# Performance work log

Measured on AMD Instinct MI355X. Metric: run time of the kernel, lower is better.

The kernel has to match this reference:

```python
import jax, jax.numpy as jnp
from jax import lax
import numpy as np

FEA = 256
NHEADS = 8
GROUPS = 32
SCALE = 1.0 / np.sqrt(FEA // NHEADS)  # 1/sqrt(qkv_dim//nheads)


def conv2d(x, w, b=None, pad=0, groups=1):
    out = lax.conv_general_dilated(
        x, w, (1, 1), [(pad, pad), (pad, pad)],
        dimension_numbers=("NCHW", "OIHW", "NCHW"),
        feature_group_count=groups)
    return out if b is None else out + b[None, :, None, None]


def group_norm(x, w, b, groups=GROUPS, eps=1e-5):
    B, C, H, W = x.shape
    xg = x.reshape(B, groups, C // groups, H, W)
    m = xg.mean(axis=(2, 3, 4), keepdims=True)
    v = xg.var(axis=(2, 3, 4), keepdims=True)
    xg = (xg - m) * lax.rsqrt(v + eps)
    return xg.reshape(B, C, H, W) * w[None, :, None, None] + b[None, :, None, None]


def l2norm(x, eps=1e-12):  # F.normalize over channel dim
    n = jnp.sqrt(jnp.sum(x * x, axis=1, keepdims=True))
    return x / jnp.maximum(n, eps)


def attn_op(q, k, v):
    b, c, xf, yf = q.shape
    sp = lambda t: t.reshape(b, NHEADS, c // NHEADS, xf * yf)
    q, k, v = sp(q), sp(k), sp(v)
    sim = jnp.einsum("bhjn,bhkn->bhjk", q, k) * SCALE  # channel attention, [b,h,c/h,c/h]
    sim = jax.nn.softmax(sim, axis=-1)
    out = jnp.einsum("bhjk,bhkn->bhjn", sim, v)
    return out.reshape(b, c, xf, yf)


def freqca(x, gn_w, gn_b, dw_w, pw_w, pw_b, ao_w, ao_b, f1_w, f2_w, f3_w, f3_b):
    H, W = x.shape[-2:]
    x = group_norm(x, gn_w, gn_b)
    qkv = conv2d(conv2d(x, dw_w, pad=1, groups=FEA), pw_w, pw_b)  # depthwise 3x3 then 1x1 -> 3*qkv_dim
    q, k, v = jnp.split(qkv, 3, axis=1)
    q, k, v = l2norm(q), l2norm(k), l2norm(v)
    qf = jnp.fft.rfft2(q, axes=(-2, -1), norm="ortho")
    kf = jnp.fft.rfft2(k, axes=(-2, -1), norm="ortho")
    vf = jnp.fft.rfft2(v, axes=(-2, -1), norm="ortho")
    amp = attn_op(jnp.abs(qf), jnp.abs(kf), jnp.abs(vf))
    phas = attn_op(jnp.angle(qf), jnp.angle(kf), jnp.angle(vf))
    out_c = amp * jnp.cos(phas) + 1j * (amp * jnp.sin(phas))  # torch.polar
    out = jnp.fft.irfft2(out_c, s=(H, W), axes=(-2, -1), norm="ortho")
    attn = conv2d(out, ao_w, ao_b) + x  # attn_res is Identity (fea_dim == dim_out)
    h = jax.nn.silu(conv2d(attn, f1_w, pad=1))
    h = conv2d(h, f2_w, pad=1)
    h = conv2d(h, f3_w, f3_b)
    return h + attn  # DropPath in eval mode = identity


def setup_inputs() -> dict:
    key = jax.random.key(0)
    ks = jax.random.split(key, 12)
    B, C, H, W = 8, FEA, 128, 128
    s = 0.02
    return {
        "x": jax.random.normal(ks[0], (B, C, H, W), jnp.float32),
        "gn_w": jnp.ones((C,), jnp.float32),
        "gn_b": jnp.zeros((C,), jnp.float32),
        "dw_w": jax.random.normal(ks[1], (C, 1, 3, 3), jnp.float32) * s,
        "pw_w": jax.random.normal(ks[2], (3 * C, C, 1, 1), jnp.float32) * s,
        "pw_b": jnp.zeros((3 * C,), jnp.float32),
        "ao_w": jax.random.normal(ks[3], (C, C, 1, 1), jnp.float32) * s,
        "ao_b": jnp.zeros((C,), jnp.float32),
        "f1_w": jax.random.normal(ks[4], (2 * C, C, 3, 3), jnp.float32) * s,
        "f2_w": jax.random.normal(ks[5], (C, 2 * C, 3, 3), jnp.float32) * s,
        "f3_w": jax.random.normal(ks[6], (C, C, 1, 1), jnp.float32) * s,
        "f3_b": jnp.zeros((C,), jnp.float32),
    }


def reference(x, gn_w, gn_b, dw_w, pw_w, pw_b, ao_w, ao_b, f1_w, f2_w, f3_w, f3_b):
    return freqca(x, gn_w, gn_b, dw_w, pw_w, pw_b, ao_w, ao_b, f1_w, f2_w, f3_w, f3_b)
```

## Files before the change

kernel.cpp:

```cpp
#include <hip/hip_runtime.h>
#include <hip/hip_bf16.h>
#include <math.h>


#define TWO_PI_D 6.283185307179586476925286766559
#define ATTN_SCALE 0.17677669529663687f

typedef __attribute__((ext_vector_type(8))) short short8;
typedef __attribute__((ext_vector_type(4))) short short4v;
typedef __attribute__((ext_vector_type(4))) float f32x4;
typedef _Float16 half8v __attribute__((ext_vector_type(8)));

__device__ inline short f2bf(float f) {
    __hip_bfloat16 h = __float2bfloat16(f);
    return *reinterpret_cast<short*>(&h);
}
__device__ inline unsigned short h_bits(_Float16 h) {
    union { _Float16 h; unsigned short u; } c; c.h = h; return c.u;
}

__global__ __launch_bounds__(256) void groupnorm_kernel(
    const float* __restrict__ x, const float* __restrict__ gw,
    const float* __restrict__ gb, float* __restrict__ out, int b0)
{
    int t = threadIdx.x;
    int lb = blockIdx.x >> 5;
    int g  = blockIdx.x & 31;
    size_t src = ((size_t)(b0 + lb) * 32 + g) * 131072;
    size_t dst = (size_t)blockIdx.x * 131072;
    const float* xp = x + src;
    double s = 0.0, ss = 0.0;
    for (int i = t; i < 131072; i += 256) { double v = xp[i]; s += v; ss += v*v; }
    __shared__ double rs[256], rss[256];
    rs[t] = s; rss[t] = ss;
    __syncthreads();
    for (int k = 128; k > 0; k >>= 1) {
        if (t < k) { rs[t] += rs[t+k]; rss[t] += rss[t+k]; }
        __syncthreads();
    }
    __shared__ float smean, sinv;
    if (t == 0) {
        double mean = rs[0] * (1.0/131072.0);
        double var  = rss[0] * (1.0/131072.0) - mean*mean;
        smean = (float)mean;
        sinv  = (float)(1.0 / sqrt(var + 1e-5));
    }
    __syncthreads();
    float mean = smean, inv = sinv;
    for (int i = t; i < 131072; i += 256) {
        int c = (g << 3) + (i >> 14);
        out[dst + i] = (xp[i] - mean) * inv * gw[c] + gb[c];
    }
}

__global__ __launch_bounds__(256) void dwconv_kernel(
    const float* __restrict__ in, const float* __restrict__ w, float* __restrict__ out)
{
    int t = threadIdx.x;
    int bc = blockIdx.x >> 6;
    int ystrip = (blockIdx.x & 63) << 1;
    int c  = bc & 255;
    const float* wp = w + c*9;
    const float* ip = in + ((size_t)bc << 14);
    __shared__ float xs[4][128];
    for (int i = t; i < 512; i += 256) {
        int rr = i >> 7, xx = i & 127;
        int yy = ystrip - 1 + rr;
        xs[rr][xx] = (yy >= 0 && yy < 128) ? ip[(yy << 7) + xx] : 0.f;
    }
    __syncthreads();
    int r0 = t >> 7;
    int x  = t & 127;
    float acc = 0.f;
    #pragma unroll
    for (int dy = 0; dy < 3; dy++) {
        const float* row = xs[r0 + dy];
        #pragma unroll
        for (int dx = 0; dx < 3; dx++) {
            int xx = x + dx - 1;
            if (xx >= 0 && xx <= 127) acc += wp[dy*3+dx] * row[xx];
        }
    }
    out[((size_t)bc << 14) + ((ystrip + r0) << 7) + x] = acc;
}

__global__ __launch_bounds__(256) void wcvtpw_kernel(
    const float* __restrict__ w, _Float16* __restrict__ whi,
    _Float16* __restrict__ wlo, int total)
{
    int i = blockIdx.x * 256 + threadIdx.x;
    if (i >= total) return;
    float v = w[i];
    _Float16 h = (_Float16)v;
    _Float16 l = (_Float16)(v - (float)h);
    whi[i] = h; wlo[i] = l;
}

__global__ __launch_bounds__(256) void twcvt_kernel(
    _Float16* __restrict__ twh, _Float16* __restrict__ twl)
{
    int i = blockIdx.x * 256 + threadIdx.x;
    if (i >= 20480) return;
    int bin = i >> 7, w = i & 127;
    double v = 0.0;
    if (bin < 65) v = cos(TWO_PI_D * ((bin * w) & 127) / 128.0) * 0.0078125;
    else if (bin < 130) v = -sin(TWO_PI_D * (((bin - 65) * w) & 127) / 128.0) * 0.0078125;
    _Float16 h = (_Float16)v;
    twh[i] = h;
    twl[i] = (_Float16)((float)v - (float)h);
}

__global__ __launch_bounds__(256) void micvt_kernel(
    _Float16* __restrict__ mih, _Float16* __restrict__ mil)
{
    int i = blockIdx.x * 256 + threadIdx.x;
    if (i >= 65536) return;
    int row = i >> 8, col = i & 255;
    int k1 = col >> 1, u = col & 1;
    int yy = row & 127;
    double ang = TWO_PI_D * ((k1 * yy) & 127) / 128.0;
    double cc = cos(ang), sn = sin(ang);
    double v;
    if (row < 128) v = (u == 0) ? cc : -sn;
    else           v = (u == 0) ? sn :  cc;
    _Float16 h = (_Float16)v;
    mih[i] = h;
    mil[i] = (_Float16)((float)v - (float)h);
}

__global__ __launch_bounds__(256) void convpw_kernel(
    const float* __restrict__ in, const _Float16* __restrict__ whi,
    const _Float16* __restrict__ wlo, const float* __restrict__ bias,
    float* __restrict__ out)
{
    int y      = blockIdx.x;
    int coBase = blockIdx.y << 7;
    int lb     = blockIdx.z;
    int t = threadIdx.x;
    int lane = t & 63;
    int wave = t >> 6;
    int wm = (wave >> 1) << 6;
    int wn = (wave & 1) << 6;
    int lr = lane & 15;
    int kg = (lane >> 4) << 3;

    __shared__ _Float16 Ah[128][40], Al[128][40];
    __shared__ _Float16 Bh[128][40], Bl[128][40];

    f32x4 acc[4][4];
    #pragma unroll
    for (int i = 0; i < 4; i++)
        #pragma unroll
        for (int j = 0; j < 4; j++) acc[i][j] = (f32x4){0.f, 0.f, 0.f, 0.f};

    const float* inrow = in + (((size_t)lb * 256) << 14) + (y << 7);
    for (int ci0 = 0; ci0 < 256; ci0 += 32) {
        __syncthreads();
        #pragma unroll
        for (int u = 0; u < 2; u++) {
            int ii = t + (u << 8);
            int co = ii >> 2, cg = ii & 3;
            *(half8v*)&Ah[co][cg << 3] =
                *(const half8v*)&whi[(size_t)(coBase + co) * 256 + ci0 + (cg << 3)];
            *(half8v*)&Al[co][cg << 3] =
                *(const half8v*)&wlo[(size_t)(coBase + co) * 256 + ci0 + (cg << 3)];
        }
        for (int i = t; i < 2048; i += 256) {
            int px = i & 127, chp = i >> 7;
            int ci = ci0 + (chp << 1);
            float v0 = inrow[((size_t)ci << 14) + px];
            float v1 = inrow[((size_t)(ci + 1) << 14) + px];
            _Float16 h0 = (_Float16)v0, h1 = (_Float16)v1;
            _Float16 l0 = (_Float16)(v0 - (float)h0);
            _Float16 l1 = (_Float16)(v1 - (float)h1);
            unsigned uh = (unsigned)h_bits(h0) | ((unsigned)h_bits(h1) << 16);
            unsigned ul = (unsigned)h_bits(l0) | ((unsigned)h_bits(l1) << 16);
            *(unsigned*)&Bh[px][chp << 1] = uh;
            *(unsigned*)&Bl[px][chp << 1] = ul;
        }
        __syncthreads();
        half8v ah[4], al[4], bh4[4], bl4[4];
        #pragma unroll
        for (int i = 0; i < 4; i++) {
            ah[i] = *(const half8v*)&Ah[wm + i*16 + lr][kg];
            al[i] = *(const half8v*)&Al[wm + i*16 + lr][kg];
        }
        #pragma unroll
        for (int j = 0; j < 4; j++) {
            bh4[j] = *(const half8v*)&Bh[wn + j*16 + lr][kg];
            bl4[j] = *(const half8v*)&Bl[wn + j*16 + lr][kg];
        }
        #pragma unroll
        for (int i = 0; i < 4; i++)
            #pragma unroll
            for (int j = 0; j < 4; j++) {
                acc[i][j] = __builtin_amdgcn_mfma_f32_16x16x32_f16(
                    ah[i], bh4[j], acc[i][j], 0, 0, 0);
                acc[i][j] = __builtin_amdgcn_mfma_f32_16x16x32_f16(
                    ah[i], bl4[j], acc[i][j], 0, 0, 0);
                acc[i][j] = __builtin_amdgcn_mfma_f32_16x16x32_f16(
                    al[i], bh4[j], acc[i][j], 0, 0, 0);
            }
    }

    int pBase = y << 7;
    int mr = (lane >> 4) << 2;
    #pragma unroll
    for (int i = 0; i < 4; i++) {
        int co0 = coBase + wm + i*16 + mr;
        #pragma unroll
        for (int j = 0; j < 4; j++) {
            int px = pBase + wn + j*16 + lr;
            #pragma unroll
            for (int r = 0; r < 4; r++) {
                out[(((size_t)(lb*768 + co0 + r)) << 14) + px] =
                    acc[i][j][r] + bias[co0 + r];
            }
        }
    }
}

__global__ __launch_bounds__(256) void l2inv_kernel(
    const float* __restrict__ qkv, float* __restrict__ invn)
{
    int p  = ((blockIdx.x & 63) << 8) + threadIdx.x;
    int bT = blockIdx.x >> 6;
    int lb = bT / 3, T = bT - 3*lb;
    const float* base = qkv + (((size_t)(lb*768 + T*256)) << 14) + p;
    double ss = 0.0;
    for (int c = 0; c < 256; c++) { double v = base[(size_t)c << 14]; ss += v*v; }
    invn[((size_t)bT << 14) + p] = 1.f / fmaxf((float)sqrt(ss), 1e-12f);
}

__global__ __launch_bounds__(256) void fftrow_mfma_kernel(
    const float* __restrict__ qkv, const float* __restrict__ invn,
    const _Float16* __restrict__ twh, const _Float16* __restrict__ twl,
    float* __restrict__ rre, float* __restrict__ rim, int chunkBase)
{
    int loc = blockIdx.x;
    int gp  = chunkBase + loc;
    int t = threadIdx.x;
    int lane = t & 63;
    int wave = t >> 6;
    int wm  = (wave >> 1) << 6;
    int wnn = (wave & 1) * 80;
    int lr = lane & 15;
    int kq = (lane >> 4) << 3;

    __shared__ _Float16 Xh[128][68], Xl[128][68];

    int lb = gp / 768, chn = gp - lb*768, T = chn >> 8;
    const float4* src = (const float4*)(qkv + ((size_t)gp << 14));
    const float4* ivp = (const float4*)(invn + (((size_t)(lb*3 + T)) << 14));

    f32x4 acc[4][5];
    #pragma unroll
    for (int i = 0; i < 4; i++)
        #pragma unroll
        for (int j = 0; j < 5; j++) acc[i][j] = (f32x4){0.f, 0.f, 0.f, 0.f};

    for (int half = 0; half < 2; half++) {
        __syncthreads();
        for (int i = t; i < 2048; i += 256) {
            int r = i >> 4, q4 = i & 15;
            int gi = (r << 5) + (half << 4) + q4;
            float4 v = src[gi], w = ivp[gi];
            v.x *= w.x; v.y *= w.y; v.z *= w.z; v.w *= w.w;
            int cl = q4 << 2;
            _Float16 h0 = (_Float16)v.x, h1 = (_Float16)v.y;
            _Float16 h2 = (_Float16)v.z, h3 = (_Float16)v.w;
            Xh[r][cl+0] = h0; Xh[r][cl+1] = h1; Xh[r][cl+2] = h2; Xh[r][cl+3] = h3;
            Xl[r][cl+0] = (_Float16)(v.x - (float)h0);
            Xl[r][cl+1] = (_Float16)(v.y - (float)h1);
            Xl[r][cl+2] = (_Float16)(v.z - (float)h2);
            Xl[r][cl+3] = (_Float16)(v.w - (float)h3);
        }
        __syncthreads();
        #pragma unroll
        for (int ks = 0; ks < 2; ks++) {
            int k0 = (ks << 5) + kq;
            int kg = (half << 6) + k0;
            half8v ah[4], al[4], bh[5], bl[5];
            #pragma unroll
            for (int i = 0; i < 4; i++) {
                ah[i] = *(const half8v*)&Xh[wm + i*16 + lr][k0];
                al[i] = *(const half8v*)&Xl[wm + i*16 + lr][k0];
            }
            #pragma unroll
            for (int j = 0; j < 5; j++) {
                int bin = wnn + j*16 + lr;
                bh[j] = *(const half8v*)&twh[(size_t)bin * 128 + kg];
                bl[j] = *(const half8v*)&twl[(size_t)bin * 128 + kg];
            }
            #pragma unroll
            for (int i = 0; i < 4; i++)
                #pragma unroll
                for (int j = 0; j < 5; j++) {
                    acc[i][j] = __builtin_amdgcn_mfma_f32_16x16x32_f16(
                        ah[i], bh[j], acc[i][j], 0, 0, 0);
                    acc[i][j] = __builtin_amdgcn_mfma_f32_16x16x32_f16(
                        al[i], bh[j], acc[i][j], 0, 0, 0);
                    acc[i][j] = __builtin_amdgcn_mfma_f32_16x16x32_f16(
                        ah[i], bl[j], acc[i][j], 0, 0, 0);
                }
        }
    }

    int mr = (lane >> 4) << 2;
    #pragma unroll
    for (int i = 0; i < 4; i++) {
        #pragma unroll
        for (int j = 0; j < 5; j++) {
            int bin = wnn + j*16 + lr;
            if (bin < 130) {
                float* dst = (bin < 65) ? rre : rim;
                int bb = (bin < 65) ? bin : bin - 65;
                #pragma unroll
                for (int r = 0; r < 4; r++) {
                    int row = wm + i*16 + mr + r;
                    dst[((size_t)loc*128 + row)*65 + bb] = acc[i][j][r];
                }
            }
        }
    }
}

__global__ __launch_bounds__(256) void fft_col_kernel(
    const float* __restrict__ rre, const float* __restrict__ rim,
    float* __restrict__ spec, int chunkBase, size_t slotStride)
{
    int kb  = blockIdx.x * 13;
    int loc = blockIdx.y;
    int gp  = chunkBase + loc;
    int t   = threadIdx.x;
    __shared__ float zr[128][14], zi[128][14];
    __shared__ float gr[8][16][14], gi[8][16][14];
    __shared__ float ct[128], st[128];
    if (t < 128) { double s, c; sincos(TWO_PI_D * t / 128.0, &s, &c);
                   st[t] = (float)s; ct[t] = (float)c; }
    for (int i = t; i < 1664; i += 256) {
        int r = i / 13, k = i - r*13;
        size_t si = ((size_t)loc*128 + r)*65 + kb + k;
        zr[r][k] = rre[si];
        zi[r][k] = rim[si];
    }
    __syncthreads();
    for (int i = t; i < 1664; i += 256) {
        int kx = i % 13, rm = i / 13;
        int r0 = rm >> 4, m = rm & 15;
        int step = (m << 3) & 127;
        float gre = 0.f, gim = 0.f;
        int idx = 0;
        for (int r1 = 0; r1 < 16; r1++) {
            float cc = ct[idx], sn = st[idx];
            float a = zr[(r1 << 3) + r0][kx], b = zi[(r1 << 3) + r0][kx];
            gre += a*cc + b*sn;
            gim += b*cc - a*sn;
            idx = (idx + step) & 127;
        }
        gr[r0][m][kx] = gre;
        gi[r0][m][kx] = gim;
    }
    __syncthreads();
    int lb = gp / 768; int chn = gp - lb*768;
    int T = chn >> 8;  int c = chn & 255;
    float* aD = spec + (size_t)(2*T)   * slotStride + ((size_t)(lb*256 + c))*8320;
    float* pD = spec + (size_t)(2*T+1) * slotStride + ((size_t)(lb*256 + c))*8320;
    for (int i = t; i < 1664; i += 256) {
        int kx = i % 13, k1 = i / 13;
        int m = k1 & 15;
        float re = 0.f, im = 0.f;
        int idx = 0;
        for (int r0 = 0; r0 < 8; r0++) {
            float cc = ct[idx], sn = st[idx];
            float a = gr[r0][m][kx], b = gi[r0][m][kx];
            re += a*cc + b*sn;
            im += b*cc - a*sn;
            idx = (idx + k1) & 127;
        }
        int kxv = kb + kx;
        if ((k1 == 0 || k1 == 64) && (kxv == 0 || kxv == 64)) im = 0.f;
        int oi = k1*65 + kxv;
        aD[oi] = sqrtf(re*re + im*im);
        pD[oi] = atan2f(im, re);
    }
}

__global__ __launch_bounds__(256) void attn_sim_kernel(
    const float* __restrict__ qA, const float* __restrict__ kA,
    float* __restrict__ simpart)
{
    int sp = blockIdx.x;
    int bh = blockIdx.y;
    int lb = bh >> 3, h = bh & 7;
    int t = threadIdx.x;
    __shared__ float qs[32][132], ks[32][132];
    const float* qb = qA + ((size_t)(lb*256 + h*32)) * 8320;
    const float* kb = kA + ((size_t)(lb*256 + h*32)) * 8320;
    float acc[4] = {0.f, 0.f, 0.f, 0.f};
    int j0 = t >> 5;
    int kq = t & 31;
    for (int sub = 0; sub < 4; sub++) {
        int n0 = sp*520 + sub*130;
        __syncthreads();
        for (int i = t; i < 4160; i += 256) {
            int j = i / 130, nn = i - j*130;
            qs[j][nn] = qb[(size_t)j*8320 + n0 + nn];
            ks[j][nn] = kb[(size_t)j*8320 + n0 + nn];
        }
        __syncthreads();
        for (int nn = 0; nn < 128; nn += 4) {
            float4 kv = *(const float4*)&ks[kq][nn];
            #pragma unroll
            for (int e = 0; e < 4; e++) {
                float4 qv = *(const float4*)&qs[j0 + e*8][nn];
                acc[e] += qv.x*kv.x + qv.y*kv.y + qv.z*kv.z + qv.w*kv.w;
            }
        }
        {
            float2 kv = *(const float2*)&ks[kq][128];
            #pragma unroll
            for (int e = 0; e < 4; e++) {
                float2 qv = *(const float2*)&qs[j0 + e*8][128];
                acc[e] += qv.x*kv.x + qv.y*kv.y;
            }
        }
    }
    float* dst = simpart + ((size_t)bh*16 + sp) * 1024;
    dst[t]       = acc[0];
    dst[t + 256] = acc[1];
    dst[t + 512] = acc[2];
    dst[t + 768] = acc[3];
}

__global__ __launch_bounds__(256) void attn_out_kernel(
    const float* __restrict__ simpart, const float* __restrict__ vA,
    float* __restrict__ outA)
{
    int nb = blockIdx.x << 8;
    int bh = blockIdx.y;
    int lb = bh >> 3, h = bh & 7;
    int t = threadIdx.x;
    __shared__ float sim[32][32];
    for (int e = t; e < 1024; e += 256) {
        float s = 0.f;
        const float* pp = simpart + (size_t)bh*16384 + e;
        #pragma unroll
        for (int sp = 0; sp < 16; sp++) s += pp[sp*1024];
        sim[e >> 5][e & 31] = s * ATTN_SCALE;
    }
    __syncthreads();
    if (t < 32) {
        float m = -1e30f;
        for (int k = 0; k < 32; k++) m = fmaxf(m, sim[t][k]);
        float s = 0.f;
        for (int k = 0; k < 32; k++) s += expf(sim[t][k] - m);
        float inv = 1.f / s;
        for (int k = 0; k < 32; k++) sim[t][k] = expf(sim[t][k] - m) * inv;
    }
    __syncthreads();
    int n = nb + t;
    if (n >= 8320) return;
    const float* vb = vA + ((size_t)(lb*256 + h*32)) * 8320 + n;
    float vv[32];
    #pragma unroll
    for (int k = 0; k < 32; k++) vv[k] = vb[(size_t)k * 8320];
    float* ob = outA + ((size_t)(lb*256 + h*32)) * 8320 + n;
    for (int j = 0; j < 32; j++) {
        float o = 0.f;
        #pragma unroll
        for (int k = 0; k < 32; k++) o += sim[j][k] * vv[k];
        ob[(size_t)j * 8320] = o;
    }
}

__global__ __launch_bounds__(256) void ifftcol_mfma_kernel(
    const float* __restrict__ ampo, const float* __restrict__ pho,
    const _Float16* __restrict__ mih, const _Float16* __restrict__ mil,
    float* __restrict__ tre, float* __restrict__ tim)
{
    int plane = blockIdx.x;
    int t = threadIdx.x;
    int lane = t & 63;
    int wave = t >> 6;
    int wm = wave << 6;
    int lr = lane & 15;
    int kg = (lane >> 4) << 3;

    __shared__ _Float16 Bh[80][72], Bl[80][72];

    const float* ab = ampo + (size_t)plane * 8320;
    const float* pb = pho  + (size_t)plane * 8320;

    f32x4 acc[4][5];
    #pragma unroll
    for (int i = 0; i < 4; i++)
        #pragma unroll
        for (int j = 0; j < 5; j++) acc[i][j] = (f32x4){0.f, 0.f, 0.f, 0.f};

    for (int kc = 0; kc < 4; kc++) {
        __syncthreads();
        for (int i = t; i < 2080; i += 256) {
            int k1l = i / 65, kx = i - k1l*65;
            int k1 = (kc << 5) + k1l;
            float a = ab[k1*65 + kx];
            float p = pb[k1*65 + kx];
            float sp, cp; sincosf(p, &sp, &cp);
            float zr = a * cp, zi = a * sp;
            _Float16 hr = (_Float16)zr, hi = (_Float16)zi;
            unsigned uh = (unsigned)h_bits(hr) | ((unsigned)h_bits(hi) << 16);
            unsigned ul = (unsigned)h_bits((_Float16)(zr - (float)hr))
                        | ((unsigned)h_bits((_Float16)(zi - (float)hi)) << 16);
            *(unsigned*)&Bh[kx][k1l << 1] = uh;
            *(unsigned*)&Bl[kx][k1l << 1] = ul;
        }
        __syncthreads();
        #pragma unroll
        for (int ks = 0; ks < 2; ks++) {
            int kq = (ks << 5) + kg;
            int kgl = (kc << 6) + kq;
            half8v ah[4], al[4], bh[5], bl[5];
            #pragma unroll
            for (int i = 0; i < 4; i++) {
                int row = wm + i*16 + lr;
                ah[i] = *(const half8v*)&mih[(size_t)row * 256 + kgl];
                al[i] = *(const half8v*)&mil[(size_t)row * 256 + kgl];
            }
            #pragma unroll
            for (int j = 0; j < 5; j++) {
                int col = j*16 + lr;
                bh[j] = *(const half8v*)&Bh[col][kq];
                bl[j] = *(const half8v*)&Bl[col][kq];
            }
            #pragma unroll
            for (int i = 0; i < 4; i++)
                #pragma unroll
                for (int j = 0; j < 5; j++) {
                    acc[i][j] = __builtin_amdgcn_mfma_f32_16x16x32_f16(
                        ah[i], bh[j], acc[i][j], 0, 0, 0);
                    acc[i][j] = __builtin_amdgcn_mfma_f32_16x16x32_f16(
                        al[i], bh[j], acc[i][j], 0, 0, 0);
                    acc[i][j] = __builtin_amdgcn_mfma_f32_16x16x32_f16(
                        ah[i], bl[j], acc[i][j], 0, 0, 0);
                }
        }
    }

    int mr = (lane >> 4) << 2;
    #pragma unroll
    for (int i = 0; i < 4; i++) {
        #pragma unroll
        for (int j = 0; j < 5; j++) {
            int col = j*16 + lr;
            if (col < 65) {
                #pragma unroll
                for (int r = 0; r < 4; r++) {
                    int row = wm + i*16 + mr + r;
                    if (row < 128)
                        tre[((size_t)plane*128 + row)*65 + col] = acc[i][j][r];
                    else
                        tim[((size_t)plane*128 + (row - 128))*65 + col] = acc[i][j][r];
                }
            }
        }
    }
}

__global__ __launch_bounds__(256) void ifft_row_kernel(
    const float* __restrict__ tre, const float* __restrict__ tim,
    float* __restrict__ spat)
{
    int rc    = blockIdx.x;
    int plane = blockIdx.y;
    int t     = threadIdx.x;
    __shared__ float tr[16][66], ti[16][66];
    __shared__ float ct[128], st[128];
    if (t < 128) { double s, c; sincos(TWO_PI_D * t / 128.0, &s, &c);
                   st[t] = (float)s; ct[t] = (float)c; }
    for (int i = t; i < 1040; i += 256) {
        int r = i / 65, k = i - r*65;
        size_t si = ((size_t)plane*128 + rc*16 + r)*65 + k;
        float sc = (k >= 1 && k < 64) ? 2.f : 1.f;
        tr[r][k] = tre[si] * sc;
        ti[r][k] = tim[si] * sc;
    }
    __syncthreads();
    for (int oo = t; oo < 260; oo += 256) {
        int x = oo % 65, rq = oo / 65;
        int r0i = rq << 2;
        float C0 = tr[r0i+0][0], C1 = tr[r0i+1][0], C2 = tr[r0i+2][0], C3 = tr[r0i+3][0];
        float S0 = 0.f, S1 = 0.f, S2 = 0.f, S3 = 0.f;
        int m = x;
        for (int k = 1; k <= 64; k++) {
            float cc = ct[m], sn = st[m];
            C0 += tr[r0i+0][k]*cc; S0 += ti[r0i+0][k]*sn;
            C1 += tr[r0i+1][k]*cc; S1 += ti[r0i+1][k]*sn;
            C2 += tr[r0i+2][k]*cc; S2 += ti[r0i+2][k]*sn;
            C3 += tr[r0i+3][k]*cc; S3 += ti[r0i+3][k]*sn;
            m = (m + x) & 127;
        }
        size_t ob = ((size_t)plane << 14) + ((rc*16 + r0i) << 7);
        spat[ob + x]       = (C0 - S0)*0.0078125f;
        spat[ob + 128 + x] = (C1 - S1)*0.0078125f;
        spat[ob + 256 + x] = (C2 - S2)*0.0078125f;
        spat[ob + 384 + x] = (C3 - S3)*0.0078125f;
        if (x >= 1 && x <= 63) {
            int xm = 128 - x;
            spat[ob + xm]       = (C0 + S0)*0.0078125f;
            spat[ob + 128 + xm] = (C1 + S1)*0.0078125f;
            spat[ob + 256 + xm] = (C2 + S2)*0.0078125f;
            spat[ob + 384 + xm] = (C3 + S3)*0.0078125f;
        }
    }
}

__global__ __launch_bounds__(256) void wcvt_kernel(
    const float* __restrict__ w, short* __restrict__ wbf,
    int Cout, int Cin, int RR)
{
    int i = blockIdx.x * 256 + threadIdx.x;
    int total = Cout * Cin * RR;
    if (i >= total) return;
    int rr = i % RR;
    int ci = (i / RR) % Cin;
    int co = i / (RR * Cin);
    wbf[((size_t)rr * Cout + co) * Cin + ci] = f2bf(w[i]);
}

__global__ __launch_bounds__(256) void convmf2_kernel(
    const float* __restrict__ in, const short* __restrict__ wbf,
    const float* __restrict__ bias, const float* __restrict__ res,
    float* __restrict__ out, short* __restrict__ out_t,
    int Cin, int Cout, int act, int in_b0, int res_b0, int out_b0)
{
    int y      = blockIdx.x;
    int coBase = blockIdx.y << 7;
    int lb = blockIdx.z;
    int t = threadIdx.x;
    int lane = t & 63;
    int wave = t >> 6;
    int wm = (wave >> 1) << 6;
    int wn = (wave & 1) << 6;

    __shared__ short As[128][40];
    __shared__ short Bs[128][40];

    f32x4 acc[4][4];
    #pragma unroll
    for (int i = 0; i < 4; i++)
        #pragma unroll
        for (int j = 0; j < 4; j++) acc[i][j] = (f32x4){0.f, 0.f, 0.f, 0.f};

    const size_t inb = ((size_t)(in_b0 + lb) * Cin) << 14;
    int lr = lane & 15;
    int kg = (lane >> 4) << 3;

    const float* inrow = in + inb + (y << 7);
    const short* wslice = wbf + (size_t)coBase * Cin;
    for (int ci0 = 0; ci0 < Cin; ci0 += 32) {
        __syncthreads();
        #pragma unroll
        for (int u = 0; u < 2; u++) {
            int ii = t + (u << 8);
            int co = ii >> 2, cg = ii & 3;
            *(short8*)&As[co][cg << 3] =
                *(const short8*)&wslice[(size_t)co * Cin + ci0 + (cg << 3)];
        }
        for (int i = t; i < 2048; i += 256) {
            int px = i & 127, chp = i >> 7;
            int ci = ci0 + (chp << 1);
            float v0 = inrow[((size_t)ci << 14) + px];
            float v1 = inrow[((size_t)(ci + 1) << 14) + px];
            unsigned u2 = (unsigned)(unsigned short)f2bf(v0)
                        | ((unsigned)(unsigned short)f2bf(v1) << 16);
            *(unsigned*)&Bs[px][chp << 1] = u2;
        }
        __syncthreads();
        short8 af[4], bf[4];
        #pragma unroll
        for (int i = 0; i < 4; i++)
            af[i] = *(const short8*)&As[wm + i*16 + lr][kg];
        #pragma unroll
        for (int j = 0; j < 4; j++)
            bf[j] = *(const short8*)&Bs[wn + j*16 + lr][kg];
        #pragma unroll
        for (int i = 0; i < 4; i++)
            #pragma unroll
            for (int j = 0; j < 4; j++)
                acc[i][j] = __builtin_amdgcn_mfma_f32_16x16x32_bf16(
                    af[i], bf[j], acc[i][j], 0, 0, 0);
    }

    int pBase = y << 7;
    int mr = (lane >> 4) << 2;
    #pragma unroll
    for (int i = 0; i < 4; i++) {
        int co0 = coBase + wm + i*16 + mr;
        #pragma unroll
        for (int j = 0; j < 4; j++) {
            int px = pBase + wn + j*16 + lr;
            float v[4];
            #pragma unroll
            for (int r = 0; r < 4; r++) {
                float vv = acc[i][j][r] + (bias ? bias[co0 + r] : 0.f);
                if (act == 1) vv = vv / (1.f + expf(-vv));
                if (res) vv += res[(((size_t)(res_b0 + lb) * Cout + co0 + r) << 14) + px];
                v[r] = vv;
            }
            if (out) {
                #pragma unroll
                for (int r = 0; r < 4; r++)
                    out[(((size_t)(out_b0 + lb) * Cout + co0 + r) << 14) + px] = v[r];
            }
            if (out_t) {
                short4v s4 = { f2bf(v[0]), f2bf(v[1]), f2bf(v[2]), f2bf(v[3]) };
                *(short4v*)&out_t[((size_t)(lb*16384 + px)) * Cout + co0] = s4;
            }
        }
    }
}

template<int R>
__global__ __launch_bounds__(256) void convmf3_kernel(
    const short* __restrict__ in_t, const short* __restrict__ wbf,
    const float* __restrict__ bias, const float* __restrict__ res,
    float* __restrict__ out, short* __restrict__ out_t,
    int Cin, int Cout, int act, int res_b0, int out_b0)
{
    int y      = blockIdx.x;
    int coBase = blockIdx.y << 7;
    int lb = blockIdx.z;
    int t = threadIdx.x;
    int lane = t & 63;
    int wave = t >> 6;
    int wm = (wave >> 1) << 6;
    int wn = (wave & 1) << 6;
    int lr = lane & 15;
    int kg = (lane >> 4) << 3;

    f32x4 acc[4][4];
    #pragma unroll
    for (int i = 0; i < 4; i++)
        #pragma unroll
        for (int j = 0; j < 4; j++) acc[i][j] = (f32x4){0.f, 0.f, 0.f, 0.f};

    const short* inb = in_t + (((size_t)lb << 14)) * Cin;
    const short8 zero8 = {0,0,0,0,0,0,0,0};

    for (int rr = 0; rr < R*R; rr++) {
        int dy = (R == 3) ? (rr / 3) : 0;
        int dx = (R == 3) ? (rr - dy*3) : 0;
        int yy = (R == 3) ? (y + dy - 1) : y;
        if (R == 3 && (yy < 0 || yy > 127)) continue;
        const short* wrow[4];
        #pragma unroll
        for (int i = 0; i < 4; i++)
            wrow[i] = wbf + ((size_t)rr * Cout + coBase) * Cin
                    + (size_t)(wm + i*16 + lr) * Cin + kg;
        const short* brow_base = inb + ((size_t)(yy << 7)) * Cin;
        const short* brow[4];
        bool bvalid[4];
        #pragma unroll
        for (int j = 0; j < 4; j++) {
            int pxl = wn + j*16 + lr;
            int xx = (R == 3) ? (pxl + dx - 1) : pxl;
            bvalid[j] = !(R == 3 && (xx < 0 || xx > 127));
            brow[j] = brow_base + (size_t)(bvalid[j] ? xx : 0) * Cin + kg;
        }
        #pragma unroll
        for (int ci0 = 0; ci0 < 512; ci0 += 32) {
            if (ci0 >= Cin) break;
            short8 af[4], bf[4];
            #pragma unroll
            for (int i = 0; i < 4; i++)
                af[i] = *(const short8*)&wrow[i][ci0];
            #pragma unroll
            for (int j = 0; j < 4; j++)
                bf[j] = bvalid[j] ? *(const short8*)&brow[j][ci0] : zero8;
            #pragma unroll
            for (int i = 0; i < 4; i++)
                #pragma unroll
                for (int j = 0; j < 4; j++)
                    acc[i][j] = __builtin_amdgcn_mfma_f32_16x16x32_bf16(
                        af[i], bf[j], acc[i][j], 0, 0, 0);
        }
    }

    int pBase = y << 7;
    int mr = (lane >> 4) << 2;
    #pragma unroll
    for (int i = 0; i < 4; i++) {
        int co0 = coBase + wm + i*16 + mr;
        #pragma unroll
        for (int j = 0; j < 4; j++) {
            int px = pBase + wn + j*16 + lr;
            float v[4];
            #pragma unroll
            for (int r = 0; r < 4; r++) {
                float vv = acc[i][j][r] + (bias ? bias[co0 + r] : 0.f);
                if (act == 1) vv = vv / (1.f + expf(-vv));
                if (res) vv += res[(((size_t)(res_b0 + lb) * Cout + co0 + r) << 14) + px];
                v[r] = vv;
            }
            if (out) {
                #pragma unroll
                for (int r = 0; r < 4; r++)
                    out[(((size_t)(out_b0 + lb) * Cout + co0 + r) << 14) + px] = v[r];
            }
            if (out_t) {
                short4v s4 = { f2bf(v[0]), f2bf(v[1]), f2bf(v[2]), f2bf(v[3]) };
                *(short4v*)&out_t[((size_t)(lb*16384 + px)) * Cout + co0] = s4;
            }
        }
    }
}

extern "C" void kernel_launch(void* const* d_in, const int* in_sizes, int n_in,
                              void* d_out, int out_size, void* d_ws, size_t ws_size,
                              hipStream_t stream) {
    (void)in_sizes; (void)n_in; (void)out_size;
    const float* x    = (const float*)d_in[0];
    const float* gn_w = (const float*)d_in[1];
    const float* gn_b = (const float*)d_in[2];
    const float* dw_w = (const float*)d_in[3];
    const float* pw_w = (const float*)d_in[4];
    const float* pw_b = (const float*)d_in[5];
    const float* ao_w = (const float*)d_in[6];
    const float* ao_b = (const float*)d_in[7];
    const float* f1_w = (const float*)d_in[8];
    const float* f2_w = (const float*)d_in[9];
    const float* f3_w = (const float*)d_in[10];
    const float* f3_b = (const float*)d_in[11];
    float* outp = (float*)d_out;

    const size_t F_QKV  = 12582912;
    const size_t F_SLOT = 2129920;
    const size_t F_SPEC = 6 * F_SLOT;
    const size_t F_XN   = 4194304;
    const size_t F_E    = 4259840;
    const size_t F_SIMP = 262144;
    const size_t F_TOT  = F_QKV + F_SPEC + F_XN + F_E + F_SIMP;
    const size_t F_WB   = 1527808;

    int NB = 0;
    for (int cand : {8, 4, 2, 1}) {
        if (((size_t)cand * F_TOT + F_WB) * 4 <= ws_size) { NB = cand; break; }
    }
    if (NB == 0) return;

    float* wsf  = (float*)d_ws;
    float* qkv  = wsf;
    short* abuf = (short*)wsf;
    short* h1t  = (short*)(wsf + (size_t)NB * 2097152);
    short* h2t  = (short*)(wsf + (size_t)NB * 6291456);
    float* spec = wsf + (size_t)NB * F_QKV;
    size_t ss   = (size_t)NB * F_SLOT;
    float* tre  = spec + 2*ss;
    float* tim  = spec + 3*ss;
    float* spat = spec + 4*ss;
    float* xn   = spec + 6*ss;
    float* ebuf = xn + (size_t)NB * F_XN;
    float* dw   = ebuf;
    float* rre  = ebuf;
    float* rim  = ebuf + (size_t)NB * 2129920;
    float* simpf = ebuf + (size_t)NB * F_E;
    float* invn  = simpf;
    float* simp  = simpf;
    short* wb    = (short*)(wsf + (size_t)NB * F_TOT);
    short* wb_ao = wb;
    short* wb_f1 = wb + 65536;
    short* wb_f2 = wb + 1245184;
    short* wb_f3 = wb + 2424832;
    _Float16* wb_pw_hi = (_Float16*)(wb + 2490368);
    _Float16* wb_pw_lo = (_Float16*)(wb + 2686976);
    _Float16* wb_tw_hi = (_Float16*)(wb + 2883584);
    _Float16* wb_tw_lo = (_Float16*)(wb + 2904064);
    _Float16* wb_mi_hi = (_Float16*)(wb + 2924544);
    _Float16* wb_mi_lo = (_Float16*)(wb + 2990080);

    wcvt_kernel<<<256,  256, 0, stream>>>(ao_w, wb_ao, 256, 256, 1);
    wcvt_kernel<<<4608, 256, 0, stream>>>(f1_w, wb_f1, 512, 256, 9);
    wcvt_kernel<<<4608, 256, 0, stream>>>(f2_w, wb_f2, 256, 512, 9);
    wcvt_kernel<<<256,  256, 0, stream>>>(f3_w, wb_f3, 256, 256, 1);
    wcvtpw_kernel<<<768, 256, 0, stream>>>(pw_w, wb_pw_hi, wb_pw_lo, 196608);
    twcvt_kernel<<<80, 256, 0, stream>>>(wb_tw_hi, wb_tw_lo);
    micvt_kernel<<<256, 256, 0, stream>>>(wb_mi_hi, wb_mi_lo);

    const int passes = 8 / NB;
    for (int p = 0; p < passes; p++) {
        int b0 = p * NB;
        groupnorm_kernel<<<NB*32, 256, 0, stream>>>(x, gn_w, gn_b, xn, b0);
        dwconv_kernel<<<NB*256*64, 256, 0, stream>>>(xn, dw_w, dw);
        convpw_kernel<<<dim3(128, 6, NB), 256, 0, stream>>>(
            dw, wb_pw_hi, wb_pw_lo, pw_b, qkv);
        l2inv_kernel<<<NB*3*64, 256, 0, stream>>>(qkv, invn);
        for (int chunk = 0; chunk < 3; chunk++) {
            fftrow_mfma_kernel<<<NB*256, 256, 0, stream>>>(
                qkv, invn, wb_tw_hi, wb_tw_lo, rre, rim, chunk*NB*256);
            fft_col_kernel<<<dim3(5, NB*256), 256, 0, stream>>>(
                rre, rim, spec, chunk*NB*256, ss);
        }
        attn_sim_kernel<<<dim3(16, NB*8), 256, 0, stream>>>(spec + 0*ss, spec + 2*ss, simp);
        attn_out_kernel<<<dim3(33, NB*8), 256, 0, stream>>>(simp, spec + 4*ss, spec + 0*ss);
        attn_sim_kernel<<<dim3(16, NB*8), 256, 0, stream>>>(spec + 1*ss, spec + 3*ss, simp);
        attn_out_kernel<<<dim3(33, NB*8), 256, 0, stream>>>(simp, spec + 5*ss, spec + 1*ss);
        ifftcol_mfma_kernel<<<NB*256, 256, 0, stream>>>(
            spec + 0*ss, spec + 1*ss, wb_mi_hi, wb_mi_lo, tre, tim);
        ifft_row_kernel<<<dim3(8, NB*256), 256, 0, stream>>>(tre, tim, spat);
        convmf2_kernel<<<dim3(128, 2, NB), 256, 0, stream>>>(
            spat, wb_ao, ao_b, xn, outp, abuf, 256, 256, 0, 0, 0, b0);
        convmf3_kernel<3><<<dim3(128, 4, NB), 256, 0, stream>>>(
            abuf, wb_f1, nullptr, nullptr, nullptr, h1t, 256, 512, 1, 0, 0);
        convmf3_kernel<3><<<dim3(128, 2, NB), 256, 0, stream>>>(
            h1t, wb_f2, nullptr, nullptr, nullptr, h2t, 512, 256, 0, 0, 0);
        convmf3_kernel<1><<<dim3(128, 2, NB), 256, 0, stream>>>(
            h2t, wb_f3, f3_b, outp, outp, nullptr, 256, 256, 0, b0, b0);
    }
}
```

Baseline: 6.176 ms.

## Replace scalar inverse row DFT with split-fp16 MFMA matmul against precomputed matrix

The inverse real row FFT, previously a scalar DFT loop over shared-memory twiddle tables, becomes a dense matmul. Each plane's 128x130 interleaved real/imag spectrum is multiplied by a precomputed 130x128 inverse-DFT matrix (Hermitian doubling and 1/128 scaling folded in) using fp16 MFMA. Precision is kept with hi/lo splitting and three MFMAs per tile. A small setup kernel builds the matrix once, and the workspace grows slightly. This trades scalar FMA work for matrix-core throughput, at the cost of padding K to 192, redundant computation of mirrored outputs, and some precision risk.

```diff
diff --git a/kernel.cpp b/kernel.cpp
--- a/kernel.cpp
+++ b/kernel.cpp
@@ -126,6 +126,24 @@
     _Float16 h = (_Float16)v;
     mih[i] = h;
     mil[i] = (_Float16)((float)v - (float)h);
+}
+
+__global__ __launch_bounds__(256) void nrcvt_kernel(
+    _Float16* __restrict__ nrh, _Float16* __restrict__ nrl)
+{
+    int i = blockIdx.x * 256 + threadIdx.x;
+    if (i >= 24576) return;
+    int x = i / 192, kk = i - x*192;
+    double v = 0.0;
+    if (kk < 130) {
+        int k = kk >> 1, u = kk & 1;
+        double sc = (k >= 1 && k < 64) ? 2.0 : 1.0;
+        double ang = TWO_PI_D * ((k * x) & 127) / 128.0;
+        v = ((u == 0) ? cos(ang) : -sin(ang)) * sc * 0.0078125;
+    }
+    _Float16 h = (_Float16)v;
+    nrh[i] = h;
+    nrl[i] = (_Float16)((float)v - (float)h);
 }
 
 __global__ __launch_bounds__(256) void convpw_kernel(
@@ -566,50 +584,88 @@
     }
 }
 
-__global__ __launch_bounds__(256) void ifft_row_kernel(
+__global__ __launch_bounds__(256) void ifftrow_mfma_kernel(
     const float* __restrict__ tre, const float* __restrict__ tim,
+    const _Float16* __restrict__ nrh, const _Float16* __restrict__ nrl,
     float* __restrict__ spat)
 {
-    int rc    = blockIdx.x;
-    int plane = blockIdx.y;
-    int t     = threadIdx.x;
-    __shared__ float tr[16][66], ti[16][66];
-    __shared__ float ct[128], st[128];
-    if (t < 128) { double s, c; sincos(TWO_PI_D * t / 128.0, &s, &c);
-                   st[t] = (float)s; ct[t] = (float)c; }
-    for (int i = t; i < 1040; i += 256) {
-        int r = i / 65, k = i - r*65;
-        size_t si = ((size_t)plane*128 + rc*16 + r)*65 + k;
-        float sc = (k >= 1 && k < 64) ? 2.f : 1.f;
-        tr[r][k] = tre[si] * sc;
-        ti[r][k] = tim[si] * sc;
-    }
-    __syncthreads();
-    for (int oo = t; oo < 260; oo += 256) {
-        int x = oo % 65, rq = oo / 65;
-        int r0i = rq << 2;
-        float C0 = tr[r0i+0][0], C1 = tr[r0i+1][0], C2 = tr[r0i+2][0], C3 = tr[r0i+3][0];
-        float S0 = 0.f, S1 = 0.f, S2 = 0.f, S3 = 0.f;
-        int m = x;
-        for (int k = 1; k <= 64; k++) {
-            float cc = ct[m], sn = st[m];
-            C0 += tr[r0i+0][k]*cc; S0 += ti[r0i+0][k]*sn;
-            C1 += tr[r0i+1][k]*cc; S1 += ti[r0i+1][k]*sn;
-            C2 += tr[r0i+2][k]*cc; S2 += ti[r0i+2][k]*sn;
-            C3 += tr[r0i+3][k]*cc; S3 += ti[r0i+3][k]*sn;
-            m = (m + x) & 127;
-        }
-        size_t ob = ((size_t)plane << 14) + ((rc*16 + r0i) << 7);
-        spat[ob + x]       = (C0 - S0)*0.0078125f;
-        spat[ob + 128 + x] = (C1 - S1)*0.0078125f;
-        spat[ob + 256 + x] = (C2 - S2)*0.0078125f;
-        spat[ob + 384 + x] = (C3 - S3)*0.0078125f;
-        if (x >= 1 && x <= 63) {
-            int xm = 128 - x;
-            spat[ob + xm]       = (C0 + S0)*0.0078125f;
-            spat[ob + 128 + xm] = (C1 + S1)*0.0078125f;
-            spat[ob + 256 + xm] = (C2 + S2)*0.0078125f;
-            spat[ob + 384 + xm] = (C3 + S3)*0.0078125f;
+    int plane = blockIdx.x;
+    int t = threadIdx.x;
+    int lane = t & 63;
+    int wave = t >> 6;
+    int wm = (wave >> 1) << 6;
+    int wn = (wave & 1) << 6;
+    int lr = lane & 15;
+    int kg = (lane >> 4) << 3;
+
+    __shared__ _Float16 Ah[128][72], Al[128][72];
+
+    const float* trb = tre + (size_t)plane * 128 * 65;
+    const float* tib = tim + (size_t)plane * 128 * 65;
+
+    f32x4 acc[4][4];
+    #pragma unroll
+    for (int i = 0; i < 4; i++)
+        #pragma unroll
+        for (int j = 0; j < 4; j++) acc[i][j] = (f32x4){0.f, 0.f, 0.f, 0.f};
+
+    for (int kc = 0; kc < 3; kc++) {
+        __syncthreads();
+        for (int i = t; i < 8192; i += 256) {
+            int r = i >> 6, kkl = i & 63;
+            int kkg = (kc << 6) + kkl;
+            float v = 0.f;
+            if (kkg < 130) {
+                int k = kkg >> 1;
+                v = (kkg & 1) ? tib[r*65 + k] : trb[r*65 + k];
+            }
+            _Float16 h = (_Float16)v;
+            Ah[r][kkl] = h;
+            Al[r][kkl] = (_Float16)(v - (float)h);
+        }
+        __syncthreads();
+        #pragma unroll
+        for (int ks = 0; ks < 2; ks++) {
+            int kq = (ks << 5) + kg;
+            int kgl = (kc << 6) + kq;
+            half8v ah[4], al[4], bh[4], bl[4];
+            #pragma unroll
+            for (int i = 0; i < 4; i++) {
+                ah[i] = *(const half8v*)&Ah[wm + i*16 + lr][kq];
+                al[i] = *(const half8v*)&Al[wm + i*16 + lr][kq];
+            }
+            #pragma unroll
+            for (int j = 0; j < 4; j++) {
+                int x = wn + j*16 + lr;
+                bh[j] = *(const half8v*)&nrh[(size_t)x * 192 + kgl];
+                bl[j] = *(const half8v*)&nrl[(size_t)x * 192 + kgl];
+            }
+            #pragma unroll
+            for (int i = 0; i < 4; i++)
+                #pragma unroll
+                for (int j = 0; j < 4; j++) {
+                    acc[i][j] = __builtin_amdgcn_mfma_f32_16x16x32_f16(
+                        ah[i], bh[j], acc[i][j], 0, 0, 0);
+                    acc[i][j] = __builtin_amdgcn_mfma_f32_16x16x32_f16(
+                        al[i], bh[j], acc[i][j], 0, 0, 0);
+                    acc[i][j] = __builtin_amdgcn_mfma_f32_16x16x32_f16(
+                        ah[i], bl[j], acc[i][j], 0, 0, 0);
+                }
+        }
+    }
+
+    int mr = (lane >> 4) << 2;
+    size_t pbase = (size_t)plane << 14;
+    #pragma unroll
+    for (int i = 0; i < 4; i++) {
+        #pragma unroll
+        for (int j = 0; j < 4; j++) {
+            int x = wn + j*16 + lr;
+            #pragma unroll
+            for (int r = 0; r < 4; r++) {
+                int row = wm + i*16 + mr + r;
+                spat[pbase + (row << 7) + x] = acc[i][j][r];
+            }
         }
     }
 }
@@ -840,7 +896,7 @@
     const size_t F_E    = 4259840;
     const size_t F_SIMP = 262144;
     const size_t F_TOT  = F_QKV + F_SPEC + F_XN + F_E + F_SIMP;
-    const size_t F_WB   = 1527808;
+    const size_t F_WB   = 1552384;
 
     int NB = 0;
     for (int cand : {8, 4, 2, 1}) {
@@ -877,6 +933,8 @@
     _Float16* wb_tw_lo = (_Float16*)(wb + 2904064);
     _Float16* wb_mi_hi = (_Float16*)(wb + 2924544);
     _Float16* wb_mi_lo = (_Float16*)(wb + 2990080);
+    _Float16* wb_nr_hi = (_Float16*)(wb + 3055616);
+    _Float16* wb_nr_lo = (_Float16*)(wb + 3080192);
 
     wcvt_kernel<<<256,  256, 0, stream>>>(ao_w, wb_ao, 256, 256, 1);
     wcvt_kernel<<<4608, 256, 0, stream>>>(f1_w, wb_f1, 512, 256, 9);
@@ -885,6 +943,7 @@
     wcvtpw_kernel<<<768, 256, 0, stream>>>(pw_w, wb_pw_hi, wb_pw_lo, 196608);
     twcvt_kernel<<<80, 256, 0, stream>>>(wb_tw_hi, wb_tw_lo);
     micvt_kernel<<<256, 256, 0, stream>>>(wb_mi_hi, wb_mi_lo);
+    nrcvt_kernel<<<96, 256, 0, stream>>>(wb_nr_hi, wb_nr_lo);
 
     const int passes = 8 / NB;
     for (int p = 0; p < passes; p++) {
@@ -906,7 +965,8 @@
         attn_out_kernel<<<dim3(33, NB*8), 256, 0, stream>>>(simp, spec + 5*ss, spec + 1*ss);
         ifftcol_mfma_kernel<<<NB*256, 256, 0, stream>>>(
             spec + 0*ss, spec + 1*ss, wb_mi_hi, wb_mi_lo, tre, tim);
-        ifft_row_kernel<<<dim3(8, NB*256), 256, 0, stream>>>(tre, tim, spat);
+        ifftrow_mfma_kernel<<<NB*256, 256, 0, stream>>>(
+            tre, tim, wb_nr_hi, wb_nr_lo, spat);
         convmf2_kernel<<<dim3(128, 2, NB), 256, 0, stream>>>(
             spat, wb_ao, ao_b, xn, outp, abuf, 256, 256, 0, 0, 0, b0);
         convmf3_kernel<3><<<dim3(128, 4, NB), 256, 0, stream>>>(
```

Result: no change. 6.133 ms (-0.7%).
